# Optimization experiments

Hardware: AMD Instinct MI355X
Metric: run time of the kernel (lower is better)

## Reference

```python
import jax, jax.numpy as jnp
import numpy as np

B, S, C, MID = 32, 8192, 256, 128

def setup_inputs() -> dict:
    key = jax.random.key(0)
    k_x, k_w1, k_b1, k_w2, k_b2 = jax.random.split(key, 5)
    bound1 = 1.0 / np.sqrt(C)
    bound2 = 1.0 / np.sqrt(MID)
    return {
        "x": jax.random.normal(k_x, (B, S, C), dtype=jnp.float32),
        "W1": jax.random.uniform(k_w1, (C, MID), jnp.float32, -bound1, bound1),
        "b1": jax.random.uniform(k_b1, (MID,), jnp.float32, -bound1, bound1),
        "w2": jax.random.uniform(k_w2, (MID,), jnp.float32, -bound2, bound2),
        "b2": jax.random.uniform(k_b2, (), jnp.float32, -bound2, bound2),
    }

def reference(x, W1, b1, w2, b2):
    # scores: (B, S) — dropout is identity in eval mode
    h = jnp.tanh(jnp.einsum("bsc,cm->bsm", x, W1) + b1)       # (B, S, MID)
    scores = jnp.einsum("bsm,m->bs", h, w2) + b2              # (B, S)
    attn = jax.nn.softmax(scores, axis=-1)                    # softmax over seq
    out = jnp.einsum("bsc,bs->bc", x, attn)                   # weighted sum over seq
    return out
```

## Files before the change

### kernel.cpp

```cpp
#include <hip/hip_runtime.h>
#include <hip/hip_bf16.h>


typedef __attribute__((ext_vector_type(8))) short short8;
typedef __attribute__((ext_vector_type(4))) float f32x4;
typedef unsigned short u16;

constexpr int Bb = 32;
constexpr int Ss = 8192;
constexpr int Cc = 256;
constexpr int MIDm = 128;
constexpr int BM = 128;
constexpr int BK = 32;
constexpr int NCH = Cc / BK;
constexpr int NBLK = Bb * Ss / BM;
constexpr int BPB = Ss / BM;

__device__ __forceinline__ u16 f2bf(float f) {
  return __builtin_bit_cast(u16, __float2bfloat16(f));
}

__global__ __launch_bounds__(256) void wprep_kernel(
    const float* __restrict__ W1, u16* __restrict__ FB)
{
  const int t    = blockIdx.x * 256 + threadIdx.x;
  const int lane = t & 63;
  const int nt   = (t >> 6) & 3;
  const int kcc  = (t >> 8) & 7;
  const int wc   = (t >> 11) & 1;
  const int n    = wc * 64 + nt * 16 + (lane & 15);
  const int k0   = kcc * 32 + (lane >> 4) * 8;
  union { u16 v[8]; short8 s; } u;
  #pragma unroll
  for (int e = 0; e < 8; ++e) u.v[e] = f2bf(W1[(size_t)(k0 + e) * MIDm + n]);
  *(short8*)(FB + (size_t)t * 8) = u.s;
}

__global__ __launch_bounds__(256, 3) void fused_kernel(
    const float* __restrict__ x, const u16* __restrict__ FB,
    const float* __restrict__ b1, const float* __restrict__ w2,
    float* __restrict__ oPart, float* __restrict__ mPart, float* __restrict__ lPart)
{
  __shared__ __align__(16) char smem[49152];
  #define SXA(buf) (smem + (buf) * 16384)
  #define SBB(buf) (smem + 32768 + (buf) * 8192)

  const int tid  = threadIdx.x;
  const int lane = tid & 63;
  const int w    = tid >> 6;
  const int wr   = w >> 1;
  const int wc   = w & 1;
  const int q    = lane >> 4;
  const int ln   = lane & 15;
  const int row0 = blockIdx.x * BM;

  f32x4 acc[4][4];
  #pragma unroll
  for (int nt = 0; nt < 4; ++nt) {
    float bj = b1[64 * wc + 16 * nt + ln];
    #pragma unroll
    for (int mt = 0; mt < 4; ++mt) {
      acc[mt][nt][0] = bj; acc[mt][nt][1] = bj; acc[mt][nt][2] = bj; acc[mt][nt][3] = bj;
    }
  }

  #define STAGE_ALL(buf, kc)                                                          \
    {                                                                                 \
      _Pragma("unroll")                                                               \
      for (int r = 0; r < 4; ++r) {                                                   \
        int L   = r * 4096 + tid * 16;                                                \
        int row = L >> 7;                                                             \
        int cb  = (L & 127) ^ ((row & 7) << 4);                                       \
        const char* src = (const char*)x                                              \
            + ((size_t)(row0 + row) * Cc + (size_t)(kc) * BK) * 4 + cb;               \
        __builtin_amdgcn_global_load_lds(                                             \
            (const __attribute__((address_space(1))) void*)src,                       \
            (__attribute__((address_space(3))) void*)(SXA(buf) + L),                  \
            16, 0, 0);                                                                \
      }                                                                               \
      _Pragma("unroll")                                                               \
      for (int r = 0; r < 2; ++r) {                                                   \
        const char* srcb = (const char*)FB                                            \
            + ((size_t)r * 2048 + (size_t)(kc) * 256) * 16 + (size_t)tid * 16;        \
        __builtin_amdgcn_global_load_lds(                                             \
            (const __attribute__((address_space(1))) void*)srcb,                      \
            (__attribute__((address_space(3))) void*)(SBB(buf) + r * 4096 + tid * 16),\
            16, 0, 0);                                                                \
      }                                                                               \
    }

  STAGE_ALL(0, 0);

  #pragma unroll
  for (int kc = 0; kc < NCH; ++kc) {
    const int cur = kc & 1;
    if (kc < NCH - 1) STAGE_ALL(1 - cur, kc + 1);

    __builtin_amdgcn_sched_barrier(0);
    if (kc < NCH - 1) asm volatile("s_waitcnt vmcnt(6)");
    else              asm volatile("s_waitcnt vmcnt(0)");
    __builtin_amdgcn_sched_barrier(0);
    __builtin_amdgcn_s_barrier();
    __builtin_amdgcn_sched_barrier(0);

    const char* bb = SBB(cur) + wc * 4096 + lane * 16;
    short8 bfrag[4];
    #pragma unroll
    for (int nt = 0; nt < 4; ++nt)
      bfrag[nt] = *(const short8*)(bb + nt * 1024);

    #pragma unroll
    for (int mt = 0; mt < 4; ++mt) {
      const int row = 64 * wr + 16 * mt + ln;
      const int s   = (row & 7) << 4;
      const char* base = SXA(cur) + row * 128;
      float4 lo = *(const float4*)(base + ((q * 32) ^ s));
      float4 hi = *(const float4*)(base + ((q * 32 + 16) ^ s));
      union { u16 v[8]; short8 s8; } t8;
      t8.v[0] = f2bf(lo.x); t8.v[1] = f2bf(lo.y); t8.v[2] = f2bf(lo.z); t8.v[3] = f2bf(lo.w);
      t8.v[4] = f2bf(hi.x); t8.v[5] = f2bf(hi.y); t8.v[6] = f2bf(hi.z); t8.v[7] = f2bf(hi.w);
      #pragma unroll
      for (int nt = 0; nt < 4; ++nt)
        acc[mt][nt] = __builtin_amdgcn_mfma_f32_16x16x32_bf16(
            t8.s8, bfrag[nt], acc[mt][nt], 0, 0, 0);
    }

    __builtin_amdgcn_sched_barrier(0);
    __builtin_amdgcn_s_barrier();
  }

  float* sScore = (float*)smem;
  float* sP     = (float*)(smem + 1024);
  float* sO     = (float*)(smem + 2048);
  float* sML    = (float*)(smem + 6144);

  float w2v[4];
  #pragma unroll
  for (int nt = 0; nt < 4; ++nt) w2v[nt] = w2[64 * wc + 16 * nt + ln];

  float p[4][4];
  #pragma unroll
  for (int mt = 0; mt < 4; ++mt)
    #pragma unroll
    for (int r = 0; r < 4; ++r) p[mt][r] = 0.f;

  #pragma unroll
  for (int mt = 0; mt < 4; ++mt)
    #pragma unroll
    for (int nt = 0; nt < 4; ++nt)
      #pragma unroll
      for (int r = 0; r < 4; ++r)
        p[mt][r] += (1.0f - 2.0f / (__expf(2.0f * acc[mt][nt][r]) + 1.0f)) * w2v[nt];

  #pragma unroll
  for (int off = 1; off < 16; off <<= 1)
    #pragma unroll
    for (int mt = 0; mt < 4; ++mt)
      #pragma unroll
      for (int r = 0; r < 4; ++r)
        p[mt][r] += __shfl_xor(p[mt][r], off);

  if (ln == 0) {
    #pragma unroll
    for (int mt = 0; mt < 4; ++mt)
      #pragma unroll
      for (int r = 0; r < 4; ++r)
        sScore[wc * BM + 64 * wr + 16 * mt + 4 * q + r] = p[mt][r];
  }
  __syncthreads();

  if (tid < BM) sP[tid] = sScore[tid] + sScore[BM + tid];
  __syncthreads();
  if (w == 0) {
    float a = sP[lane], b = sP[lane + 64];
    float m = fmaxf(a, b);
    #pragma unroll
    for (int off = 1; off < 64; off <<= 1) m = fmaxf(m, __shfl_xor(m, off));
    float e0 = __expf(a - m), e1 = __expf(b - m);
    sP[lane] = e0; sP[lane + 64] = e1;
    float s = e0 + e1;
    #pragma unroll
    for (int off = 1; off < 64; off <<= 1) s += __shfl_xor(s, off);
    if (lane == 0) { sML[0] = m; sML[1] = s; }
  }
  __syncthreads();

  const int c4 = tid & 63;
  const int rg = tid >> 6;
  const float* xo = x + (size_t)(row0 + rg * 32) * Cc + c4 * 4;
  float4 o = make_float4(0.f, 0.f, 0.f, 0.f);
  #pragma unroll 8
  for (int r = 0; r < 32; ++r) {
    float pw = sP[rg * 32 + r];
    float4 xv = *(const float4*)(xo + (size_t)r * Cc);
    o.x = fmaf(pw, xv.x, o.x);
    o.y = fmaf(pw, xv.y, o.y);
    o.z = fmaf(pw, xv.z, o.z);
    o.w = fmaf(pw, xv.w, o.w);
  }
  *(float4*)&sO[rg * Cc + c4 * 4] = o;
  __syncthreads();

  float oc = sO[tid] + sO[Cc + tid] + sO[2 * Cc + tid] + sO[3 * Cc + tid];
  oPart[(size_t)blockIdx.x * Cc + tid] = oc;
  if (tid == 0) { mPart[blockIdx.x] = sML[0]; lPart[blockIdx.x] = sML[1]; }
}

__global__ __launch_bounds__(256) void combine_kernel(
    const float* __restrict__ oPart, const float* __restrict__ mPart,
    const float* __restrict__ lPart, float* __restrict__ out)
{
  const int b = blockIdx.x;
  const int t = threadIdx.x;
  float M = -3.4e38f;
  for (int k = 0; k < BPB; ++k) M = fmaxf(M, mPart[b * BPB + k]);
  float num = 0.f, den = 0.f;
  for (int k = 0; k < BPB; ++k) {
    float wgt = __expf(mPart[b * BPB + k] - M);
    den += wgt * lPart[b * BPB + k];
    num = fmaf(wgt, oPart[(size_t)(b * BPB + k) * Cc + t], num);
  }
  out[b * Cc + t] = num / den;
}

extern "C" void kernel_launch(void* const* d_in, const int* in_sizes, int n_in,
                              void* d_out, int out_size, void* d_ws, size_t ws_size,
                              hipStream_t stream)
{
  const float* x  = (const float*)d_in[0];
  const float* W1 = (const float*)d_in[1];
  const float* b1 = (const float*)d_in[2];
  const float* w2 = (const float*)d_in[3];
  float* out = (float*)d_out;

  u16*   FB    = (u16*)d_ws;
  float* oPart = (float*)((char*)d_ws + 65536);
  float* mPart = (float*)((char*)d_ws + 65536 + 2097152);
  float* lPart = (float*)((char*)d_ws + 65536 + 2097152 + 8192);

  wprep_kernel<<<16, 256, 0, stream>>>(W1, FB);
  fused_kernel<<<NBLK, 256, 0, stream>>>(x, FB, b1, w2, oPart, mPart, lPart);
  combine_kernel<<<Bb, Cc, 0, stream>>>(oPart, mPart, lPart, out);
}
```

Baseline: 95.36 us.

## Keep W1 fragments in registers and stream full-width row slabs of x

Each wave now owns a 32-column slice of MID and holds all of its bf16 W1 fragments in registers for the whole K range. The B operand no longer goes through LDS each chunk. The x tile is staged as four 32-row full-K slabs (32KB each, double-buffered in 64KB LDS) instead of eight 32-column K chunks, which halves the number of barriers. Score reduction now sums four per-wave partials. The cost is higher register and LDS use, with occupancy lowered from 3 to 2 blocks per CU.

```diff
diff --git a/kernel.cpp b/kernel.cpp
--- a/kernel.cpp
+++ b/kernel.cpp
@@ -11,8 +11,6 @@
 constexpr int Cc = 256;
 constexpr int MIDm = 128;
 constexpr int BM = 128;
-constexpr int BK = 32;
-constexpr int NCH = Cc / BK;
 constexpr int NBLK = Bb * Ss / BM;
 constexpr int BPB = Ss / BM;
 
@@ -25,10 +23,10 @@
 {
   const int t    = blockIdx.x * 256 + threadIdx.x;
   const int lane = t & 63;
-  const int nt   = (t >> 6) & 3;
-  const int kcc  = (t >> 8) & 7;
-  const int wc   = (t >> 11) & 1;
-  const int n    = wc * 64 + nt * 16 + (lane & 15);
+  const int nt   = (t >> 6) & 1;
+  const int kcc  = (t >> 7) & 7;
+  const int wc   = (t >> 10) & 3;
+  const int n    = wc * 32 + nt * 16 + (lane & 15);
   const int k0   = kcc * 32 + (lane >> 4) * 8;
   union { u16 v[8]; short8 s; } u;
   #pragma unroll
@@ -36,93 +34,93 @@
   *(short8*)(FB + (size_t)t * 8) = u.s;
 }
 
-__global__ __launch_bounds__(256, 3) void fused_kernel(
+__global__ __launch_bounds__(256, 2) void fused_kernel(
     const float* __restrict__ x, const u16* __restrict__ FB,
     const float* __restrict__ b1, const float* __restrict__ w2,
     float* __restrict__ oPart, float* __restrict__ mPart, float* __restrict__ lPart)
 {
-  __shared__ __align__(16) char smem[49152];
-  #define SXA(buf) (smem + (buf) * 16384)
-  #define SBB(buf) (smem + 32768 + (buf) * 8192)
-
+  __shared__ __align__(16) char smem[65536];
   const int tid  = threadIdx.x;
   const int lane = tid & 63;
   const int w    = tid >> 6;
-  const int wr   = w >> 1;
-  const int wc   = w & 1;
   const int q    = lane >> 4;
   const int ln   = lane & 15;
   const int row0 = blockIdx.x * BM;
 
-  f32x4 acc[4][4];
-  #pragma unroll
-  for (int nt = 0; nt < 4; ++nt) {
-    float bj = b1[64 * wc + 16 * nt + ln];
-    #pragma unroll
-    for (int mt = 0; mt < 4; ++mt) {
-      acc[mt][nt][0] = bj; acc[mt][nt][1] = bj; acc[mt][nt][2] = bj; acc[mt][nt][3] = bj;
-    }
-  }
-
-  #define STAGE_ALL(buf, kc)                                                          \
+  short8 Bf[8][2];
+  {
+    const u16* fbw = FB + ((size_t)(w * 8) * 2 + 0) * 64 * 8;
+    #pragma unroll
+    for (int kcc = 0; kcc < 8; ++kcc)
+      #pragma unroll
+      for (int nt = 0; nt < 2; ++nt)
+        Bf[kcc][nt] = *(const short8*)(FB +
+            ((size_t)(((w * 8 + kcc) * 2 + nt) * 64 + lane)) * 8);
+    (void)fbw;
+  }
+
+  f32x4 acc[4][2][2];
+  #pragma unroll
+  for (int nt = 0; nt < 2; ++nt) {
+    float bj = b1[32 * w + 16 * nt + ln];
+    #pragma unroll
+    for (int sl = 0; sl < 4; ++sl)
+      #pragma unroll
+      for (int mt = 0; mt < 2; ++mt) {
+        acc[sl][mt][nt][0] = bj; acc[sl][mt][nt][1] = bj;
+        acc[sl][mt][nt][2] = bj; acc[sl][mt][nt][3] = bj;
+      }
+  }
+
+  #define STAGE(buf, sl)                                                              \
     {                                                                                 \
       _Pragma("unroll")                                                               \
-      for (int r = 0; r < 4; ++r) {                                                   \
-        int L   = r * 4096 + tid * 16;                                                \
-        int row = L >> 7;                                                             \
-        int cb  = (L & 127) ^ ((row & 7) << 4);                                       \
+      for (int r = 0; r < 8; ++r) {                                                   \
+        int L     = r * 4096 + tid * 16;                                              \
+        int row   = L >> 10;                                                          \
+        int inrow = (L & 1023) ^ ((row & 7) << 4);                                    \
         const char* src = (const char*)x                                              \
-            + ((size_t)(row0 + row) * Cc + (size_t)(kc) * BK) * 4 + cb;               \
+            + (size_t)(row0 + (sl) * 32 + row) * 1024 + inrow;                        \
         __builtin_amdgcn_global_load_lds(                                             \
             (const __attribute__((address_space(1))) void*)src,                       \
-            (__attribute__((address_space(3))) void*)(SXA(buf) + L),                  \
-            16, 0, 0);                                                                \
-      }                                                                               \
-      _Pragma("unroll")                                                               \
-      for (int r = 0; r < 2; ++r) {                                                   \
-        const char* srcb = (const char*)FB                                            \
-            + ((size_t)r * 2048 + (size_t)(kc) * 256) * 16 + (size_t)tid * 16;        \
-        __builtin_amdgcn_global_load_lds(                                             \
-            (const __attribute__((address_space(1))) void*)srcb,                      \
-            (__attribute__((address_space(3))) void*)(SBB(buf) + r * 4096 + tid * 16),\
+            (__attribute__((address_space(3))) void*)(smem + (buf) * 32768 + L),      \
             16, 0, 0);                                                                \
       }                                                                               \
     }
 
-  STAGE_ALL(0, 0);
-
-  #pragma unroll
-  for (int kc = 0; kc < NCH; ++kc) {
-    const int cur = kc & 1;
-    if (kc < NCH - 1) STAGE_ALL(1 - cur, kc + 1);
-
-    __builtin_amdgcn_sched_barrier(0);
-    if (kc < NCH - 1) asm volatile("s_waitcnt vmcnt(6)");
-    else              asm volatile("s_waitcnt vmcnt(0)");
+  STAGE(0, 0);
+
+  #pragma unroll
+  for (int sl = 0; sl < 4; ++sl) {
+    const int cur = sl & 1;
+    if (sl < 3) STAGE(1 - cur, sl + 1);
+
+    __builtin_amdgcn_sched_barrier(0);
+    if (sl < 3) asm volatile("s_waitcnt vmcnt(8)" ::: "memory");
+    else        asm volatile("s_waitcnt vmcnt(0)" ::: "memory");
     __builtin_amdgcn_sched_barrier(0);
     __builtin_amdgcn_s_barrier();
     __builtin_amdgcn_sched_barrier(0);
 
-    const char* bb = SBB(cur) + wc * 4096 + lane * 16;
-    short8 bfrag[4];
-    #pragma unroll
-    for (int nt = 0; nt < 4; ++nt)
-      bfrag[nt] = *(const short8*)(bb + nt * 1024);
-
-    #pragma unroll
-    for (int mt = 0; mt < 4; ++mt) {
-      const int row = 64 * wr + 16 * mt + ln;
-      const int s   = (row & 7) << 4;
-      const char* base = SXA(cur) + row * 128;
-      float4 lo = *(const float4*)(base + ((q * 32) ^ s));
-      float4 hi = *(const float4*)(base + ((q * 32 + 16) ^ s));
-      union { u16 v[8]; short8 s8; } t8;
-      t8.v[0] = f2bf(lo.x); t8.v[1] = f2bf(lo.y); t8.v[2] = f2bf(lo.z); t8.v[3] = f2bf(lo.w);
-      t8.v[4] = f2bf(hi.x); t8.v[5] = f2bf(hi.y); t8.v[6] = f2bf(hi.z); t8.v[7] = f2bf(hi.w);
-      #pragma unroll
-      for (int nt = 0; nt < 4; ++nt)
-        acc[mt][nt] = __builtin_amdgcn_mfma_f32_16x16x32_bf16(
-            t8.s8, bfrag[nt], acc[mt][nt], 0, 0, 0);
+    const char* bufb = smem + cur * 32768;
+    #pragma unroll
+    for (int kcc = 0; kcc < 8; ++kcc) {
+      #pragma unroll
+      for (int mt = 0; mt < 2; ++mt) {
+        const int row = 16 * mt + ln;
+        const int sw  = (row & 7) << 4;
+        const char* base = bufb + row * 1024;
+        const int off = kcc * 128 + q * 32;
+        float4 lo = *(const float4*)(base + (off ^ sw));
+        float4 hi = *(const float4*)(base + ((off + 16) ^ sw));
+        union { u16 v[8]; short8 s8; } t8;
+        t8.v[0] = f2bf(lo.x); t8.v[1] = f2bf(lo.y); t8.v[2] = f2bf(lo.z); t8.v[3] = f2bf(lo.w);
+        t8.v[4] = f2bf(hi.x); t8.v[5] = f2bf(hi.y); t8.v[6] = f2bf(hi.z); t8.v[7] = f2bf(hi.w);
+        #pragma unroll
+        for (int nt = 0; nt < 2; ++nt)
+          acc[sl][mt][nt] = __builtin_amdgcn_mfma_f32_16x16x32_bf16(
+              t8.s8, Bf[kcc][nt], acc[sl][mt][nt], 0, 0, 0);
+      }
     }
 
     __builtin_amdgcn_sched_barrier(0);
@@ -130,46 +128,40 @@
   }
 
   float* sScore = (float*)smem;
-  float* sP     = (float*)(smem + 1024);
-  float* sO     = (float*)(smem + 2048);
-  float* sML    = (float*)(smem + 6144);
-
-  float w2v[4];
-  #pragma unroll
-  for (int nt = 0; nt < 4; ++nt) w2v[nt] = w2[64 * wc + 16 * nt + ln];
-
-  float p[4][4];
-  #pragma unroll
-  for (int mt = 0; mt < 4; ++mt)
-    #pragma unroll
-    for (int r = 0; r < 4; ++r) p[mt][r] = 0.f;
-
-  #pragma unroll
-  for (int mt = 0; mt < 4; ++mt)
-    #pragma unroll
-    for (int nt = 0; nt < 4; ++nt)
-      #pragma unroll
-      for (int r = 0; r < 4; ++r)
-        p[mt][r] += (1.0f - 2.0f / (__expf(2.0f * acc[mt][nt][r]) + 1.0f)) * w2v[nt];
-
-  #pragma unroll
-  for (int off = 1; off < 16; off <<= 1)
-    #pragma unroll
-    for (int mt = 0; mt < 4; ++mt)
-      #pragma unroll
-      for (int r = 0; r < 4; ++r)
-        p[mt][r] += __shfl_xor(p[mt][r], off);
-
-  if (ln == 0) {
-    #pragma unroll
-    for (int mt = 0; mt < 4; ++mt)
-      #pragma unroll
-      for (int r = 0; r < 4; ++r)
-        sScore[wc * BM + 64 * wr + 16 * mt + 4 * q + r] = p[mt][r];
-  }
-  __syncthreads();
-
-  if (tid < BM) sP[tid] = sScore[tid] + sScore[BM + tid];
+  float* sP     = (float*)(smem + 2048);
+  float* sO     = (float*)(smem + 2560);
+  float* sML    = (float*)(smem + 6656);
+
+  float w2v[2];
+  #pragma unroll
+  for (int nt = 0; nt < 2; ++nt) w2v[nt] = w2[32 * w + 16 * nt + ln];
+
+  #pragma unroll
+  for (int sl = 0; sl < 4; ++sl)
+    #pragma unroll
+    for (int mt = 0; mt < 2; ++mt) {
+      float p[4];
+      #pragma unroll
+      for (int r = 0; r < 4; ++r) p[r] = 0.f;
+      #pragma unroll
+      for (int nt = 0; nt < 2; ++nt)
+        #pragma unroll
+        for (int r = 0; r < 4; ++r)
+          p[r] += (1.0f - 2.0f / (__expf(2.0f * acc[sl][mt][nt][r]) + 1.0f)) * w2v[nt];
+      #pragma unroll
+      for (int off = 1; off < 16; off <<= 1)
+        #pragma unroll
+        for (int r = 0; r < 4; ++r) p[r] += __shfl_xor(p[r], off);
+      if (ln == 0) {
+        #pragma unroll
+        for (int r = 0; r < 4; ++r)
+          sScore[w * BM + 32 * sl + 16 * mt + 4 * q + r] = p[r];
+      }
+    }
+  __syncthreads();
+
+  if (tid < BM)
+    sP[tid] = sScore[tid] + sScore[BM + tid] + sScore[2 * BM + tid] + sScore[3 * BM + tid];
   __syncthreads();
   if (w == 0) {
     float a = sP[lane], b = sP[lane + 64];
```

New measurement: 102.3 us. 7.2% more time.

## Halve row tile to 64, raise occupancy, and parallelize combine across channels

Applied to the files above, without the earlier changes.

Shrinks the per-block row tile from 128 to 64 rows, halving accumulators and LDS per block so four blocks can reside per CU, and doubles the grid to 4096 blocks. The combine kernel is split across 8 channel groups with a split-k reduction through shared memory, giving 256 blocks instead of 32. The cost is that each block still reloads the full W1 fragment buffer for half as many rows, doubling B-operand traffic, and partial outputs grow twice as large.

```diff
diff --git a/kernel.cpp b/kernel.cpp
--- a/kernel.cpp
+++ b/kernel.cpp
@@ -10,7 +10,7 @@
 constexpr int Ss = 8192;
 constexpr int Cc = 256;
 constexpr int MIDm = 128;
-constexpr int BM = 128;
+constexpr int BM = 64;
 constexpr int BK = 32;
 constexpr int NCH = Cc / BK;
 constexpr int NBLK = Bb * Ss / BM;
@@ -36,14 +36,17 @@
   *(short8*)(FB + (size_t)t * 8) = u.s;
 }
 
-__global__ __launch_bounds__(256, 3) void fused_kernel(
+__global__ __launch_bounds__(256, 4) void fused_kernel(
     const float* __restrict__ x, const u16* __restrict__ FB,
     const float* __restrict__ b1, const float* __restrict__ w2,
     float* __restrict__ oPart, float* __restrict__ mPart, float* __restrict__ lPart)
 {
-  __shared__ __align__(16) char smem[49152];
-  #define SXA(buf) (smem + (buf) * 16384)
-  #define SBB(buf) (smem + 32768 + (buf) * 8192)
+  __shared__ __align__(16) char sXA[2][8192];
+  __shared__ __align__(16) char sB[2][8192];
+  __shared__ float sScore[2][BM];
+  __shared__ float sP[BM];
+  __shared__ float sO[4][Cc];
+  __shared__ float sML[2];
 
   const int tid  = threadIdx.x;
   const int lane = tid & 63;
@@ -54,12 +57,12 @@
   const int ln   = lane & 15;
   const int row0 = blockIdx.x * BM;
 
-  f32x4 acc[4][4];
+  f32x4 acc[2][4];
   #pragma unroll
   for (int nt = 0; nt < 4; ++nt) {
-    float bj = b1[64 * wc + 16 * nt + ln];
-    #pragma unroll
-    for (int mt = 0; mt < 4; ++mt) {
+    float bj = b1[wc * 64 + nt * 16 + ln];
+    #pragma unroll
+    for (int mt = 0; mt < 2; ++mt) {
       acc[mt][nt][0] = bj; acc[mt][nt][1] = bj; acc[mt][nt][2] = bj; acc[mt][nt][3] = bj;
     }
   }
@@ -67,7 +70,7 @@
   #define STAGE_ALL(buf, kc)                                                          \
     {                                                                                 \
       _Pragma("unroll")                                                               \
-      for (int r = 0; r < 4; ++r) {                                                   \
+      for (int r = 0; r < 2; ++r) {                                                   \
         int L   = r * 4096 + tid * 16;                                                \
         int row = L >> 7;                                                             \
         int cb  = (L & 127) ^ ((row & 7) << 4);                                       \
@@ -75,7 +78,7 @@
             + ((size_t)(row0 + row) * Cc + (size_t)(kc) * BK) * 4 + cb;               \
         __builtin_amdgcn_global_load_lds(                                             \
             (const __attribute__((address_space(1))) void*)src,                       \
-            (__attribute__((address_space(3))) void*)(SXA(buf) + L),                  \
+            (__attribute__((address_space(3))) void*)(&sXA[buf][0] + L),              \
             16, 0, 0);                                                                \
       }                                                                               \
       _Pragma("unroll")                                                               \
@@ -84,7 +87,7 @@
             + ((size_t)r * 2048 + (size_t)(kc) * 256) * 16 + (size_t)tid * 16;        \
         __builtin_amdgcn_global_load_lds(                                             \
             (const __attribute__((address_space(1))) void*)srcb,                      \
-            (__attribute__((address_space(3))) void*)(SBB(buf) + r * 4096 + tid * 16),\
+            (__attribute__((address_space(3))) void*)(&sB[buf][0] + r * 4096 + tid * 16),\
             16, 0, 0);                                                                \
       }                                                                               \
     }
@@ -97,23 +100,23 @@
     if (kc < NCH - 1) STAGE_ALL(1 - cur, kc + 1);
 
     __builtin_amdgcn_sched_barrier(0);
-    if (kc < NCH - 1) asm volatile("s_waitcnt vmcnt(6)");
-    else              asm volatile("s_waitcnt vmcnt(0)");
+    if (kc < NCH - 1) asm volatile("s_waitcnt vmcnt(4)" ::: "memory");
+    else              asm volatile("s_waitcnt vmcnt(0)" ::: "memory");
     __builtin_amdgcn_sched_barrier(0);
     __builtin_amdgcn_s_barrier();
     __builtin_amdgcn_sched_barrier(0);
 
-    const char* bb = SBB(cur) + wc * 4096 + lane * 16;
+    const char* bb = &sB[cur][0] + wc * 4096 + lane * 16;
     short8 bfrag[4];
     #pragma unroll
     for (int nt = 0; nt < 4; ++nt)
       bfrag[nt] = *(const short8*)(bb + nt * 1024);
 
     #pragma unroll
-    for (int mt = 0; mt < 4; ++mt) {
-      const int row = 64 * wr + 16 * mt + ln;
+    for (int mt = 0; mt < 2; ++mt) {
+      const int row = 32 * wr + 16 * mt + ln;
       const int s   = (row & 7) << 4;
-      const char* base = SXA(cur) + row * 128;
+      const char* base = &sXA[cur][0] + row * 128;
       float4 lo = *(const float4*)(base + ((q * 32) ^ s));
       float4 hi = *(const float4*)(base + ((q * 32 + 16) ^ s));
       union { u16 v[8]; short8 s8; } t8;
@@ -129,23 +132,18 @@
     __builtin_amdgcn_s_barrier();
   }
 
-  float* sScore = (float*)smem;
-  float* sP     = (float*)(smem + 1024);
-  float* sO     = (float*)(smem + 2048);
-  float* sML    = (float*)(smem + 6144);
-
   float w2v[4];
   #pragma unroll
-  for (int nt = 0; nt < 4; ++nt) w2v[nt] = w2[64 * wc + 16 * nt + ln];
-
-  float p[4][4];
-  #pragma unroll
-  for (int mt = 0; mt < 4; ++mt)
+  for (int nt = 0; nt < 4; ++nt) w2v[nt] = w2[wc * 64 + nt * 16 + ln];
+
+  float p[2][4];
+  #pragma unroll
+  for (int mt = 0; mt < 2; ++mt)
     #pragma unroll
     for (int r = 0; r < 4; ++r) p[mt][r] = 0.f;
 
   #pragma unroll
-  for (int mt = 0; mt < 4; ++mt)
+  for (int mt = 0; mt < 2; ++mt)
     #pragma unroll
     for (int nt = 0; nt < 4; ++nt)
       #pragma unroll
@@ -155,54 +153,52 @@
   #pragma unroll
   for (int off = 1; off < 16; off <<= 1)
     #pragma unroll
-    for (int mt = 0; mt < 4; ++mt)
+    for (int mt = 0; mt < 2; ++mt)
       #pragma unroll
       for (int r = 0; r < 4; ++r)
         p[mt][r] += __shfl_xor(p[mt][r], off);
 
   if (ln == 0) {
     #pragma unroll
-    for (int mt = 0; mt < 4; ++mt)
+    for (int mt = 0; mt < 2; ++mt)
       #pragma unroll
       for (int r = 0; r < 4; ++r)
-        sScore[wc * BM + 64 * wr + 16 * mt + 4 * q + r] = p[mt][r];
-  }
-  __syncthreads();
-
-  if (tid < BM) sP[tid] = sScore[tid] + sScore[BM + tid];
+        sScore[wc][32 * wr + 16 * mt + 4 * q + r] = p[mt][r];
+  }
+  __syncthreads();
+
+  if (tid < BM) sP[tid] = sScore[0][tid] + sScore[1][tid];
   __syncthreads();
   if (w == 0) {
-    float a = sP[lane], b = sP[lane + 64];
-    float m = fmaxf(a, b);
+    float v = sP[lane];
+    float m = v;
     #pragma unroll
     for (int off = 1; off < 64; off <<= 1) m = fmaxf(m, __shfl_xor(m, off));
-    float e0 = __expf(a - m), e1 = __expf(b - m);
-    sP[lane] = e0; sP[lane + 64] = e1;
-    float s = e0 + e1;
+    float e = __expf(v - m);
+    float s = e;
     #pragma unroll
     for (int off = 1; off < 64; off <<= 1) s += __shfl_xor(s, off);
+    sP[lane] = e;
     if (lane == 0) { sML[0] = m; sML[1] = s; }
   }
   __syncthreads();
 
-  const int c4 = tid & 63;
-  const int rg = tid >> 6;
-  const float* xo = x + (size_t)(row0 + rg * 32) * Cc + c4 * 4;
+  const float* xo = x + (size_t)(row0 + w * 16) * Cc + lane * 4;
   float4 o = make_float4(0.f, 0.f, 0.f, 0.f);
   #pragma unroll 8
-  for (int r = 0; r < 32; ++r) {
-    float pw = sP[rg * 32 + r];
+  for (int r = 0; r < 16; ++r) {
+    float pw = sP[w * 16 + r];
     float4 xv = *(const float4*)(xo + (size_t)r * Cc);
     o.x = fmaf(pw, xv.x, o.x);
     o.y = fmaf(pw, xv.y, o.y);
     o.z = fmaf(pw, xv.z, o.z);
     o.w = fmaf(pw, xv.w, o.w);
   }
-  *(float4*)&sO[rg * Cc + c4 * 4] = o;
-  __syncthreads();
-
-  float oc = sO[tid] + sO[Cc + tid] + sO[2 * Cc + tid] + sO[3 * Cc + tid];
-  oPart[(size_t)blockIdx.x * Cc + tid] = oc;
+  *(float4*)&sO[w][lane * 4] = o;
+  __syncthreads();
+
+  oPart[(size_t)blockIdx.x * Cc + tid] =
+      sO[0][tid] + sO[1][tid] + sO[2][tid] + sO[3][tid];
   if (tid == 0) { mPart[blockIdx.x] = sML[0]; lPart[blockIdx.x] = sML[1]; }
 }
 
@@ -210,17 +206,34 @@
     const float* __restrict__ oPart, const float* __restrict__ mPart,
     const float* __restrict__ lPart, float* __restrict__ out)
 {
-  const int b = blockIdx.x;
-  const int t = threadIdx.x;
+  const int b   = blockIdx.x >> 3;
+  const int cg  = blockIdx.x & 7;
+  const int kk  = threadIdx.x >> 5;
+  const int c   = threadIdx.x & 31;
+  const int col = cg * 32 + c;
+
   float M = -3.4e38f;
   for (int k = 0; k < BPB; ++k) M = fmaxf(M, mPart[b * BPB + k]);
-  float num = 0.f, den = 0.f;
-  for (int k = 0; k < BPB; ++k) {
+  float den = 0.f;
+  for (int k = 0; k < BPB; ++k)
+    den += __expf(mPart[b * BPB + k] - M) * lPart[b * BPB + k];
+
+  float num = 0.f;
+  #pragma unroll 4
+  for (int j = 0; j < BPB / 8; ++j) {
+    const int k = j * 8 + kk;
     float wgt = __expf(mPart[b * BPB + k] - M);
-    den += wgt * lPart[b * BPB + k];
-    num = fmaf(wgt, oPart[(size_t)(b * BPB + k) * Cc + t], num);
-  }
-  out[b * Cc + t] = num / den;
+    num = fmaf(wgt, oPart[(size_t)(b * BPB + k) * Cc + col], num);
+  }
+  __shared__ float red[8][32];
+  red[kk][c] = num;
+  __syncthreads();
+  if (kk == 0) {
+    float s = 0.f;
+    #pragma unroll
+    for (int i = 0; i < 8; ++i) s += red[i][c];
+    out[b * Cc + col] = s / den;
+  }
 }
 
 extern "C" void kernel_launch(void* const* d_in, const int* in_sizes, int n_in,
@@ -235,10 +248,10 @@
 
   u16*   FB    = (u16*)d_ws;
   float* oPart = (float*)((char*)d_ws + 65536);
-  float* mPart = (float*)((char*)d_ws + 65536 + 2097152);
-  float* lPart = (float*)((char*)d_ws + 65536 + 2097152 + 8192);
+  float* mPart = (float*)((char*)d_ws + 65536 + 4194304);
+  float* lPart = (float*)((char*)d_ws + 65536 + 4194304 + 16384);
 
   wprep_kernel<<<16, 256, 0, stream>>>(W1, FB);
   fused_kernel<<<NBLK, 256, 0, stream>>>(x, FB, b1, w2, oPart, mPart, lPart);
-  combine_kernel<<<Bb, Cc, 0, stream>>>(oPart, mPart, lPart, out);
-}
+  combine_kernel<<<Bb * 8, 256, 0, stream>>>(oPart, mPart, lPart, out);
+}
```

New measurement: 98.72 us. 3.5% more time.
